# Optimization experiments

Measured on AMD Instinct MI355X. Metric: run time of the kernel, lower is better.

## Reference

```python
import jax, jax.numpy as jnp
import numpy as np

N = 50000
E = 800000
IN_CH = 128
HID = 16
HEADS = 8
OUT_CH = 64
NEG_SLOPE = 0.2


def setup_inputs() -> dict:
    key = jax.random.key(0)
    ks = jax.random.split(key, 16)
    x = jax.random.normal(ks[0], (N, IN_CH), dtype=jnp.float32)
    edge_index = jax.random.randint(ks[1], (2, E), 0, N, dtype=jnp.int64)
    s = 0.05
    # GATv2 layer 1: in=128 -> heads=8, out=16 (concat -> 128)
    W1l = jax.random.normal(ks[2], (IN_CH, HEADS * HID), dtype=jnp.float32) * s
    b1l = jnp.zeros((HEADS * HID,), dtype=jnp.float32)
    W1r = jax.random.normal(ks[3], (IN_CH, HEADS * HID), dtype=jnp.float32) * s
    b1r = jnp.zeros((HEADS * HID,), dtype=jnp.float32)
    att1 = jax.random.normal(ks[4], (HEADS, HID), dtype=jnp.float32) * s
    bias1 = jnp.zeros((HEADS * HID,), dtype=jnp.float32)
    # GATv2 layer 2: in=128 -> heads=1, out=64
    W2l = jax.random.normal(ks[5], (HEADS * HID, OUT_CH), dtype=jnp.float32) * s
    b2l = jnp.zeros((OUT_CH,), dtype=jnp.float32)
    W2r = jax.random.normal(ks[6], (HEADS * HID, OUT_CH), dtype=jnp.float32) * s
    b2r = jnp.zeros((OUT_CH,), dtype=jnp.float32)
    att2 = jax.random.normal(ks[7], (1, OUT_CH), dtype=jnp.float32) * s
    bias2 = jnp.zeros((OUT_CH,), dtype=jnp.float32)
    return dict(x=x, edge_index=edge_index,
                W1l=W1l, b1l=b1l, W1r=W1r, b1r=b1r, att1=att1, bias1=bias1,
                W2l=W2l, b2l=b2l, W2r=W2r, b2r=b2r, att2=att2, bias2=bias2)


def gatv2_conv(x, src, dst, Wl, bl, Wr, br, att, bias, heads, out_ch, concat):
    n = x.shape[0]
    xl = (x @ Wl + bl).reshape(n, heads, out_ch)  # source transform
    xr = (x @ Wr + br).reshape(n, heads, out_ch)  # target transform
    m = xl[src] + xr[dst]                          # [E, H, C]
    m = jnp.where(m > 0, m, NEG_SLOPE * m)         # LeakyReLU(0.2)
    alpha = jnp.einsum('ehc,hc->eh', m, att)       # [E, H]
    # segment softmax over destination nodes (every node has a self loop)
    amax = jax.ops.segment_max(alpha, dst, num_segments=n)
    ea = jnp.exp(alpha - amax[dst])
    denom = jax.ops.segment_sum(ea, dst, num_segments=n)
    w = ea / denom[dst]                            # [E, H]
    out = jax.ops.segment_sum(xl[src] * w[:, :, None], dst, num_segments=n)
    if concat:
        out = out.reshape(n, heads * out_ch)
    else:
        out = out.mean(axis=1)
    return out + bias


def reference(x, edge_index, W1l, b1l, W1r, b1r, att1, bias1,
              W2l, b2l, W2r, b2r, att2, bias2):
    n = x.shape[0]
    loops = jnp.arange(n, dtype=edge_index.dtype)
    src = jnp.concatenate([edge_index[0], loops])
    dst = jnp.concatenate([edge_index[1], loops])
    # dropout layers are identity in eval mode
    h = gatv2_conv(x, src, dst, W1l, b1l, W1r, b1r, att1, bias1,
                   heads=HEADS, out_ch=HID, concat=True)
    h = jax.nn.elu(h)
    out = gatv2_conv(h, src, dst, W2l, b2l, W2r, b2r, att2, bias2,
                     heads=1, out_ch=OUT_CH, concat=True)
    return out
```

## Files before the change

### kernel.cpp

```cpp
#include <hip/hip_runtime.h>
#include <hip/hip_bf16.h>

constexpr int N_  = 50000;
constexpr int E_  = 800000;
constexpr int ET_ = 850000;
constexpr float NEG_SLOPE = 0.2f;

constexpr int SCAN_NB = (N_ + 255) / 256;

typedef __attribute__((ext_vector_type(8))) short short8;
typedef __attribute__((ext_vector_type(4))) float f32x4;

__device__ inline void edge_sd(int e, const int* __restrict__ ei, int& s, int& d) {
    if (e < E_) { s = ei[e]; d = ei[E_ + e]; }
    else        { s = e - E_; d = s; }
}

__device__ inline float leaky(float v) { return fmaxf(v, NEG_SLOPE * v); }

__device__ inline unsigned bf16rn(float f) {
    union { float f; unsigned u; } v; v.f = f;
    return (v.u + 0x7fffu + ((v.u >> 16) & 1u)) >> 16;
}
__device__ inline float2 unpack2(unsigned u) {
    return make_float2(__uint_as_float(u << 16), __uint_as_float(u & 0xffff0000u));
}

__global__ __launch_bounds__(256) void hist_kernel(
        const int* __restrict__ ei, int* __restrict__ count, int* __restrict__ off) {
    int e = blockIdx.x * 256 + threadIdx.x;
    if (e >= ET_) return;
    int s, d; edge_sd(e, ei, s, d);
    off[e] = atomicAdd(&count[d], 1);
}

__global__ __launch_bounds__(256) void scan_partial(
        const int* __restrict__ count, int* __restrict__ bsum) {
    __shared__ int red[256];
    int t = threadIdx.x;
    int i = blockIdx.x * 256 + t;
    red[t] = (i < N_) ? count[i] : 0;
    __syncthreads();
    #pragma unroll
    for (int o = 128; o > 0; o >>= 1) {
        if (t < o) red[t] += red[t + o];
        __syncthreads();
    }
    if (t == 0) bsum[blockIdx.x] = red[0];
}

__global__ __launch_bounds__(256) void scan_top(
        const int* __restrict__ bsum, int* __restrict__ bstart) {
    __shared__ int buf[256];
    int t = threadIdx.x;
    int v = (t < SCAN_NB) ? bsum[t] : 0;
    buf[t] = v;
    __syncthreads();
    #pragma unroll
    for (int o = 1; o < 256; o <<= 1) {
        int add = (t >= o) ? buf[t - o] : 0;
        __syncthreads();
        buf[t] += add;
        __syncthreads();
    }
    if (t < SCAN_NB) bstart[t] = buf[t] - v;
}

__global__ __launch_bounds__(256) void scan_final(
        const int* __restrict__ count, const int* __restrict__ bstart,
        int* __restrict__ start) {
    __shared__ int buf[256];
    int t = threadIdx.x;
    int i = blockIdx.x * 256 + t;
    int v = (i < N_) ? count[i] : 0;
    buf[t] = v;
    __syncthreads();
    #pragma unroll
    for (int o = 1; o < 256; o <<= 1) {
        int add = (t >= o) ? buf[t - o] : 0;
        __syncthreads();
        buf[t] += add;
        __syncthreads();
    }
    if (i < N_) start[i] = bstart[blockIdx.x] + buf[t] - v;
}

__global__ __launch_bounds__(256) void scatter_kernel(
        const int* __restrict__ ei, const int* __restrict__ start,
        const int* __restrict__ off, int* __restrict__ csr_src) {
    int e = blockIdx.x * 256 + threadIdx.x;
    if (e >= ET_) return;
    int s, d; edge_sd(e, ei, s, d);
    csr_src[start[d] + off[e]] = s;
}

__global__ __launch_bounds__(256) void convert_w(
        const float* __restrict__ Wl, const float* __restrict__ Wr,
        unsigned short* __restrict__ wsw) {
    int tid = blockIdx.x * 256 + threadIdx.x;
    if (tid >= 32768) return;
    int j    = tid & 7;
    int lane = (tid >> 3) & 63;
    int ks   = (tid >> 9) & 3;
    int ct   = tid >> 11;
    int k = ks * 32 + ((lane >> 4) & 3) * 8 + j;
    int c = ct * 16 + (lane & 15);
    float v = (c < 128) ? Wl[k * 128 + c] : Wr[k * 128 + (c - 128)];
    wsw[tid] = (unsigned short)bf16rn(v);
}

__global__ __launch_bounds__(256) void convert_w2(
        const float* __restrict__ Wl, const float* __restrict__ Wr,
        unsigned short* __restrict__ wsw2) {
    int tid = blockIdx.x * 256 + threadIdx.x;
    if (tid >= 16384) return;
    int j    = tid & 7;
    int lane = (tid >> 3) & 63;
    int ks   = (tid >> 9) & 3;
    int ct   = tid >> 11;
    int k = ks * 32 + ((lane >> 4) & 3) * 8 + j;
    int c = ct * 16 + (lane & 15);
    float v = (c < 64) ? Wl[k * 64 + c] : Wr[k * 64 + (c - 64)];
    wsw2[tid] = (unsigned short)bf16rn(v);
}

__global__ __launch_bounds__(256) void gemm1_mfma(
        const float* __restrict__ x,
        const unsigned short* __restrict__ wsw,
        const float* __restrict__ bl, const float* __restrict__ br,
        unsigned short* __restrict__ xlu, float* __restrict__ xr1) {
    const int wave = threadIdx.x >> 6;
    const int lane = threadIdx.x & 63;
    const int n0 = blockIdx.x * 16;
    const int m = lane & 15;
    const int q = (lane >> 4) & 3;
    const float* __restrict__ arow = x + (size_t)(n0 + m) * 128 + q * 8;
    short8 afrag[4];
    #pragma unroll
    for (int ks = 0; ks < 4; ++ks) {
        float4 v0 = *(const float4*)(arow + ks * 32);
        float4 v1 = *(const float4*)(arow + ks * 32 + 4);
        short8 a;
        a[0] = (short)bf16rn(v0.x); a[1] = (short)bf16rn(v0.y);
        a[2] = (short)bf16rn(v0.z); a[3] = (short)bf16rn(v0.w);
        a[4] = (short)bf16rn(v1.x); a[5] = (short)bf16rn(v1.y);
        a[6] = (short)bf16rn(v1.z); a[7] = (short)bf16rn(v1.w);
        afrag[ks] = a;
    }
    #pragma unroll
    for (int i = 0; i < 4; ++i) {
        const int ct = wave * 4 + i;
        f32x4 acc = {0.f, 0.f, 0.f, 0.f};
        #pragma unroll
        for (int ks = 0; ks < 4; ++ks) {
            short8 b = *(const short8*)(wsw + ((size_t)(ct * 4 + ks) * 64 + lane) * 8);
            acc = __builtin_amdgcn_mfma_f32_16x16x32_bf16(afrag[ks], b, acc, 0, 0, 0);
        }
        const int col = ct * 16 + m;
        if (ct < 8) {
            float bias = bl[col];
            #pragma unroll
            for (int j = 0; j < 4; ++j) {
                int row = n0 + q * 4 + j;
                xlu[(size_t)row * 128 + col] = (unsigned short)bf16rn(acc[j] + bias);
            }
        } else {
            float bias = br[col - 128];
            #pragma unroll
            for (int j = 0; j < 4; ++j) {
                int row = n0 + q * 4 + j;
                xr1[(size_t)row * 128 + (col - 128)] = acc[j] + bias;
            }
        }
    }
}

__global__ __launch_bounds__(256) void fused1(
        const int* __restrict__ csr_src, const int* __restrict__ start,
        const int* __restrict__ count,
        const unsigned* __restrict__ xl1b, const float* __restrict__ xr1,
        const float* __restrict__ att, const float* __restrict__ bias1,
        float* __restrict__ hout) {
    int t = blockIdx.x * 256 + threadIdx.x;
    int n = __builtin_amdgcn_readfirstlane(t >> 6);
    int lane = t & 63;
    if (n >= N_) return;
    float2 xr = *(const float2*)(xr1 + (size_t)n * 128 + 2 * lane);
    float2 av = *(const float2*)(att + 2 * lane);
    int p0 = __builtin_amdgcn_readfirstlane(start[n]);
    int p1 = p0 + __builtin_amdgcn_readfirstlane(count[n]);
    float2 acc = make_float2(0.f, 0.f);
    float l = 0.f;
    for (int p = p0; p < p1; p += 4) {
        int q1 = p + 1 < p1 ? p + 1 : p1 - 1;
        int q2 = p + 2 < p1 ? p + 2 : p1 - 1;
        int q3 = p + 3 < p1 ? p + 3 : p1 - 1;
        int s0 = __builtin_amdgcn_readfirstlane(csr_src[p]);
        int s1 = __builtin_amdgcn_readfirstlane(csr_src[q1]);
        int s2 = __builtin_amdgcn_readfirstlane(csr_src[q2]);
        int s3 = __builtin_amdgcn_readfirstlane(csr_src[q3]);
        float2 x0 = unpack2(xl1b[(size_t)s0 * 64 + lane]);
        float2 x1 = unpack2(xl1b[(size_t)s1 * 64 + lane]);
        float2 x2 = unpack2(xl1b[(size_t)s2 * 64 + lane]);
        float2 x3 = unpack2(xl1b[(size_t)s3 * 64 + lane]);
        float a0 = fmaf(leaky(x0.x + xr.x), av.x, leaky(x0.y + xr.y) * av.y);
        float a1 = fmaf(leaky(x1.x + xr.x), av.x, leaky(x1.y + xr.y) * av.y);
        float a2 = fmaf(leaky(x2.x + xr.x), av.x, leaky(x2.y + xr.y) * av.y);
        float a3 = fmaf(leaky(x3.x + xr.x), av.x, leaky(x3.y + xr.y) * av.y);
        a0 += __shfl_xor(a0, 1); a1 += __shfl_xor(a1, 1);
        a2 += __shfl_xor(a2, 1); a3 += __shfl_xor(a3, 1);
        a0 += __shfl_xor(a0, 2); a1 += __shfl_xor(a1, 2);
        a2 += __shfl_xor(a2, 2); a3 += __shfl_xor(a3, 2);
        a0 += __shfl_xor(a0, 4); a1 += __shfl_xor(a1, 4);
        a2 += __shfl_xor(a2, 4); a3 += __shfl_xor(a3, 4);
        float w0 = __expf(a0);
        float w1 = p + 1 < p1 ? __expf(a1) : 0.f;
        float w2 = p + 2 < p1 ? __expf(a2) : 0.f;
        float w3 = p + 3 < p1 ? __expf(a3) : 0.f;
        acc.x = fmaf(w0, x0.x, acc.x); acc.y = fmaf(w0, x0.y, acc.y); l += w0;
        acc.x = fmaf(w1, x1.x, acc.x); acc.y = fmaf(w1, x1.y, acc.y); l += w1;
        acc.x = fmaf(w2, x2.x, acc.x); acc.y = fmaf(w2, x2.y, acc.y); l += w2;
        acc.x = fmaf(w3, x3.x, acc.x); acc.y = fmaf(w3, x3.y, acc.y); l += w3;
    }
    float2 bv = *(const float2*)(bias1 + 2 * lane);
    float vx = acc.x / l + bv.x;
    float vy = acc.y / l + bv.y;
    float2 o;
    o.x = vx > 0.f ? vx : (__expf(vx) - 1.f);
    o.y = vy > 0.f ? vy : (__expf(vy) - 1.f);
    *(float2*)(hout + (size_t)n * 128 + 2 * lane) = o;
}

__global__ __launch_bounds__(256) void gemm2_mfma(
        const float* __restrict__ hbuf,
        const unsigned short* __restrict__ wsw2,
        const float* __restrict__ bl, const float* __restrict__ br,
        unsigned short* __restrict__ xlu2, float* __restrict__ xr2) {
    const int wave = threadIdx.x >> 6;
    const int lane = threadIdx.x & 63;
    const int n0 = blockIdx.x * 16;
    const int m = lane & 15;
    const int q = (lane >> 4) & 3;
    const float* __restrict__ arow = hbuf + (size_t)(n0 + m) * 128 + q * 8;
    short8 afrag[4];
    #pragma unroll
    for (int ks = 0; ks < 4; ++ks) {
        float4 v0 = *(const float4*)(arow + ks * 32);
        float4 v1 = *(const float4*)(arow + ks * 32 + 4);
        short8 a;
        a[0] = (short)bf16rn(v0.x); a[1] = (short)bf16rn(v0.y);
        a[2] = (short)bf16rn(v0.z); a[3] = (short)bf16rn(v0.w);
        a[4] = (short)bf16rn(v1.x); a[5] = (short)bf16rn(v1.y);
        a[6] = (short)bf16rn(v1.z); a[7] = (short)bf16rn(v1.w);
        afrag[ks] = a;
    }
    #pragma unroll
    for (int i = 0; i < 2; ++i) {
        const int ct = wave * 2 + i;
        f32x4 acc = {0.f, 0.f, 0.f, 0.f};
        #pragma unroll
        for (int ks = 0; ks < 4; ++ks) {
            short8 b = *(const short8*)(wsw2 + ((size_t)(ct * 4 + ks) * 64 + lane) * 8);
            acc = __builtin_amdgcn_mfma_f32_16x16x32_bf16(afrag[ks], b, acc, 0, 0, 0);
        }
        const int col = ct * 16 + m;
        if (ct < 4) {
            float bias = bl[col];
            #pragma unroll
            for (int j = 0; j < 4; ++j) {
                int row = n0 + q * 4 + j;
                xlu2[(size_t)row * 64 + col] = (unsigned short)bf16rn(acc[j] + bias);
            }
        } else {
            float bias = br[col - 64];
            #pragma unroll
            for (int j = 0; j < 4; ++j) {
                int row = n0 + q * 4 + j;
                xr2[(size_t)row * 64 + (col - 64)] = acc[j] + bias;
            }
        }
    }
}

__global__ __launch_bounds__(256) void fused2(
        const int* __restrict__ csr_src, const int* __restrict__ start,
        const int* __restrict__ count,
        const unsigned* __restrict__ xl2b, const float* __restrict__ xr2,
        const float* __restrict__ att, const float* __restrict__ bias2,
        float* __restrict__ out) {
    int t = blockIdx.x * 256 + threadIdx.x;
    int n = __builtin_amdgcn_readfirstlane(t >> 6);
    int lane = t & 63;
    int half = lane >> 5;
    int lc   = lane & 31;
    if (n >= N_) return;
    float2 xr = *(const float2*)(xr2 + (size_t)n * 64 + 2 * lc);
    float2 av = *(const float2*)(att + 2 * lc);
    int p0 = __builtin_amdgcn_readfirstlane(start[n]);
    int p1 = p0 + __builtin_amdgcn_readfirstlane(count[n]);
    float2 acc = make_float2(0.f, 0.f);
    float l = 0.f;
    for (int p = p0; p < p1; p += 8) {
        #pragma unroll
        for (int u = 0; u < 4; ++u) {
            int pe = p + 2 * u + half;
            int pc = pe < p1 ? pe : p1 - 1;
            int s  = csr_src[pc];
            float2 xv = unpack2(xl2b[(size_t)s * 32 + lc]);
            float a = fmaf(leaky(xv.x + xr.x), av.x, leaky(xv.y + xr.y) * av.y);
            a += __shfl_xor(a, 1);
            a += __shfl_xor(a, 2);
            a += __shfl_xor(a, 4);
            a += __shfl_xor(a, 8);
            a += __shfl_xor(a, 16);
            float w = pe < p1 ? __expf(a) : 0.f;
            acc.x = fmaf(w, xv.x, acc.x);
            acc.y = fmaf(w, xv.y, acc.y);
            l += w;
        }
    }
    acc.x += __shfl_xor(acc.x, 32);
    acc.y += __shfl_xor(acc.y, 32);
    l     += __shfl_xor(l, 32);
    if (half == 0) {
        float2 bv = *(const float2*)(bias2 + 2 * lc);
        float2 o;
        o.x = acc.x / l + bv.x;
        o.y = acc.y / l + bv.y;
        *(float2*)(out + (size_t)n * 64 + 2 * lc) = o;
    }
}

extern "C" void kernel_launch(void* const* d_in, const int* in_sizes, int n_in,
                              void* d_out, int out_size, void* d_ws, size_t ws_size,
                              hipStream_t stream) {
    (void)in_sizes; (void)n_in; (void)out_size; (void)ws_size;
    const float* x     = (const float*)d_in[0];
    const int*   ei    = (const int*)d_in[1];
    const float* W1l   = (const float*)d_in[2];
    const float* b1l   = (const float*)d_in[3];
    const float* W1r   = (const float*)d_in[4];
    const float* b1r   = (const float*)d_in[5];
    const float* att1  = (const float*)d_in[6];
    const float* bias1 = (const float*)d_in[7];
    const float* W2l   = (const float*)d_in[8];
    const float* b2l   = (const float*)d_in[9];
    const float* W2r   = (const float*)d_in[10];
    const float* b2r   = (const float*)d_in[11];
    const float* att2  = (const float*)d_in[12];
    const float* bias2 = (const float*)d_in[13];
    float* out = (float*)d_out;

    float* xr1      = (float*)d_ws;
    float* hbuf     = xr1 + 6400000;
    unsigned* xl1b  = (unsigned*)(hbuf + 6400000);
    int* count   = (int*)(xl1b + 3200000);
    int* startp  = count + 50000;
    int* off     = startp + 50000;
    int* csr_src = off + 850000;
    int* bsum    = csr_src + 850000;
    int* bstart  = bsum + 256;
    unsigned short* wsw2 = (unsigned short*)(bstart + 256);
    unsigned* xl2b = xl1b;
    float* xr2     = xr1;
    unsigned short* wsw = (unsigned short*)hbuf;

    hipMemsetAsync((void*)count, 0, 50000 * sizeof(int), stream);

    const int EB = (ET_ + 255) / 256;
    hist_kernel <<<EB, 256, 0, stream>>>(ei, count, off);
    scan_partial<<<SCAN_NB, 256, 0, stream>>>(count, bsum);
    scan_top    <<<1, 256, 0, stream>>>(bsum, bstart);
    scan_final  <<<SCAN_NB, 256, 0, stream>>>(count, bstart, startp);
    scatter_kernel<<<EB, 256, 0, stream>>>(ei, startp, off, csr_src);

    convert_w  <<<128, 256, 0, stream>>>(W1l, W1r, wsw);
    convert_w2 <<<64, 256, 0, stream>>>(W2l, W2r, wsw2);
    gemm1_mfma <<<N_ / 16, 256, 0, stream>>>(x, wsw, b1l, b1r,
                                             (unsigned short*)xl1b, xr1);
    fused1<<<(N_ * 64 + 255) / 256, 256, 0, stream>>>(csr_src, startp, count,
                                                      xl1b, xr1, att1, bias1, hbuf);

    gemm2_mfma <<<N_ / 16, 256, 0, stream>>>(hbuf, wsw2, b2l, b2r,
                                             (unsigned short*)xl2b, xr2);
    fused2<<<(N_ * 64 + 255) / 256, 256, 0, stream>>>(csr_src, startp, count,
                                                      xl2b, xr2, att2, bias2, out);
}
```

Measured before the change: 274.9 us.

## Pad CSR rows to multiples of eight for vectorized neighbor index loads

Each node's CSR segment is padded to a multiple of eight entries (zero-filled via an enlarged memset), so the aggregation kernels can load source indices with aligned int4 vector loads instead of clamped scalar loads. fused2 now loads all eight indices per iteration up front. The hist kernel skips the unneeded source read, and the two weight-conversion kernels are merged into one launch. The cost is a larger memset and extra padded index storage; padded slots point at node 0 and are masked by the existing weight predicates.

```diff
diff --git a/kernel.cpp b/kernel.cpp
--- a/kernel.cpp
+++ b/kernel.cpp
@@ -7,14 +7,10 @@
 constexpr float NEG_SLOPE = 0.2f;
 
 constexpr int SCAN_NB = (N_ + 255) / 256;
+constexpr int CSR_CAP = 1250008;
 
 typedef __attribute__((ext_vector_type(8))) short short8;
 typedef __attribute__((ext_vector_type(4))) float f32x4;
-
-__device__ inline void edge_sd(int e, const int* __restrict__ ei, int& s, int& d) {
-    if (e < E_) { s = ei[e]; d = ei[E_ + e]; }
-    else        { s = e - E_; d = s; }
-}
 
 __device__ inline float leaky(float v) { return fmaxf(v, NEG_SLOPE * v); }
 
@@ -30,7 +26,7 @@
         const int* __restrict__ ei, int* __restrict__ count, int* __restrict__ off) {
     int e = blockIdx.x * 256 + threadIdx.x;
     if (e >= ET_) return;
-    int s, d; edge_sd(e, ei, s, d);
+    int d = (e < E_) ? ei[E_ + e] : e - E_;
     off[e] = atomicAdd(&count[d], 1);
 }
 
@@ -39,7 +35,7 @@
     __shared__ int red[256];
     int t = threadIdx.x;
     int i = blockIdx.x * 256 + t;
-    red[t] = (i < N_) ? count[i] : 0;
+    red[t] = (i < N_) ? ((count[i] + 7) & ~7) : 0;
     __syncthreads();
     #pragma unroll
     for (int o = 128; o > 0; o >>= 1) {
@@ -72,7 +68,7 @@
     __shared__ int buf[256];
     int t = threadIdx.x;
     int i = blockIdx.x * 256 + t;
-    int v = (i < N_) ? count[i] : 0;
+    int v = (i < N_) ? ((count[i] + 7) & ~7) : 0;
     buf[t] = v;
     __syncthreads();
     #pragma unroll
@@ -90,38 +86,38 @@
         const int* __restrict__ off, int* __restrict__ csr_src) {
     int e = blockIdx.x * 256 + threadIdx.x;
     if (e >= ET_) return;
-    int s, d; edge_sd(e, ei, s, d);
+    int s, d;
+    if (e < E_) { s = ei[e]; d = ei[E_ + e]; }
+    else        { s = e - E_; d = s; }
     csr_src[start[d] + off[e]] = s;
 }
 
-__global__ __launch_bounds__(256) void convert_w(
-        const float* __restrict__ Wl, const float* __restrict__ Wr,
-        unsigned short* __restrict__ wsw) {
+__global__ __launch_bounds__(256) void convert_w_all(
+        const float* __restrict__ W1l, const float* __restrict__ W1r,
+        const float* __restrict__ W2l, const float* __restrict__ W2r,
+        unsigned short* __restrict__ wsw, unsigned short* __restrict__ wsw2) {
     int tid = blockIdx.x * 256 + threadIdx.x;
-    if (tid >= 32768) return;
-    int j    = tid & 7;
-    int lane = (tid >> 3) & 63;
-    int ks   = (tid >> 9) & 3;
-    int ct   = tid >> 11;
-    int k = ks * 32 + ((lane >> 4) & 3) * 8 + j;
-    int c = ct * 16 + (lane & 15);
-    float v = (c < 128) ? Wl[k * 128 + c] : Wr[k * 128 + (c - 128)];
-    wsw[tid] = (unsigned short)bf16rn(v);
-}
-
-__global__ __launch_bounds__(256) void convert_w2(
-        const float* __restrict__ Wl, const float* __restrict__ Wr,
-        unsigned short* __restrict__ wsw2) {
-    int tid = blockIdx.x * 256 + threadIdx.x;
-    if (tid >= 16384) return;
-    int j    = tid & 7;
-    int lane = (tid >> 3) & 63;
-    int ks   = (tid >> 9) & 3;
-    int ct   = tid >> 11;
-    int k = ks * 32 + ((lane >> 4) & 3) * 8 + j;
-    int c = ct * 16 + (lane & 15);
-    float v = (c < 64) ? Wl[k * 64 + c] : Wr[k * 64 + (c - 64)];
-    wsw2[tid] = (unsigned short)bf16rn(v);
+    if (tid >= 49152) return;
+    if (tid < 32768) {
+        int j    = tid & 7;
+        int lane = (tid >> 3) & 63;
+        int ks   = (tid >> 9) & 3;
+        int ct   = tid >> 11;
+        int k = ks * 32 + ((lane >> 4) & 3) * 8 + j;
+        int c = ct * 16 + (lane & 15);
+        float v = (c < 128) ? W1l[k * 128 + c] : W1r[k * 128 + (c - 128)];
+        wsw[tid] = (unsigned short)bf16rn(v);
+    } else {
+        int t2   = tid - 32768;
+        int j    = t2 & 7;
+        int lane = (t2 >> 3) & 63;
+        int ks   = (t2 >> 9) & 3;
+        int ct   = t2 >> 11;
+        int k = ks * 32 + ((lane >> 4) & 3) * 8 + j;
+        int c = ct * 16 + (lane & 15);
+        float v = (c < 64) ? W2l[k * 64 + c] : W2r[k * 64 + (c - 64)];
+        wsw2[t2] = (unsigned short)bf16rn(v);
+    }
 }
 
 __global__ __launch_bounds__(256) void gemm1_mfma(
@@ -192,13 +188,11 @@
     float2 acc = make_float2(0.f, 0.f);
     float l = 0.f;
     for (int p = p0; p < p1; p += 4) {
-        int q1 = p + 1 < p1 ? p + 1 : p1 - 1;
-        int q2 = p + 2 < p1 ? p + 2 : p1 - 1;
-        int q3 = p + 3 < p1 ? p + 3 : p1 - 1;
-        int s0 = __builtin_amdgcn_readfirstlane(csr_src[p]);
-        int s1 = __builtin_amdgcn_readfirstlane(csr_src[q1]);
-        int s2 = __builtin_amdgcn_readfirstlane(csr_src[q2]);
-        int s3 = __builtin_amdgcn_readfirstlane(csr_src[q3]);
+        int4 si = *(const int4*)(csr_src + p);
+        int s0 = __builtin_amdgcn_readfirstlane(si.x);
+        int s1 = __builtin_amdgcn_readfirstlane(si.y);
+        int s2 = __builtin_amdgcn_readfirstlane(si.z);
+        int s3 = __builtin_amdgcn_readfirstlane(si.w);
         float2 x0 = unpack2(xl1b[(size_t)s0 * 64 + lane]);
         float2 x1 = unpack2(xl1b[(size_t)s1 * 64 + lane]);
         float2 x2 = unpack2(xl1b[(size_t)s2 * 64 + lane]);
@@ -301,11 +295,21 @@
     float2 acc = make_float2(0.f, 0.f);
     float l = 0.f;
     for (int p = p0; p < p1; p += 8) {
+        int4 ia = *(const int4*)(csr_src + p);
+        int4 ib = *(const int4*)(csr_src + p + 4);
+        int sx[8];
+        sx[0] = __builtin_amdgcn_readfirstlane(ia.x);
+        sx[1] = __builtin_amdgcn_readfirstlane(ia.y);
+        sx[2] = __builtin_amdgcn_readfirstlane(ia.z);
+        sx[3] = __builtin_amdgcn_readfirstlane(ia.w);
+        sx[4] = __builtin_amdgcn_readfirstlane(ib.x);
+        sx[5] = __builtin_amdgcn_readfirstlane(ib.y);
+        sx[6] = __builtin_amdgcn_readfirstlane(ib.z);
+        sx[7] = __builtin_amdgcn_readfirstlane(ib.w);
         #pragma unroll
         for (int u = 0; u < 4; ++u) {
             int pe = p + 2 * u + half;
-            int pc = pe < p1 ? pe : p1 - 1;
-            int s  = csr_src[pc];
+            int s  = sx[2 * u + half];
             float2 xv = unpack2(xl2b[(size_t)s * 32 + lc]);
             float a = fmaf(leaky(xv.x + xr.x), av.x, leaky(xv.y + xr.y) * av.y);
             a += __shfl_xor(a, 1);
@@ -355,17 +359,17 @@
     float* hbuf     = xr1 + 6400000;
     unsigned* xl1b  = (unsigned*)(hbuf + 6400000);
     int* count   = (int*)(xl1b + 3200000);
-    int* startp  = count + 50000;
+    int* csr_src = count + 50000;
+    int* startp  = csr_src + CSR_CAP;
     int* off     = startp + 50000;
-    int* csr_src = off + 850000;
-    int* bsum    = csr_src + 850000;
+    int* bsum    = off + 850000;
     int* bstart  = bsum + 256;
     unsigned short* wsw2 = (unsigned short*)(bstart + 256);
     unsigned* xl2b = xl1b;
     float* xr2     = xr1;
     unsigned short* wsw = (unsigned short*)hbuf;
 
-    hipMemsetAsync((void*)count, 0, 50000 * sizeof(int), stream);
+    hipMemsetAsync((void*)count, 0, (size_t)(50000 + CSR_CAP) * 4, stream);
 
     const int EB = (ET_ + 255) / 256;
     hist_kernel <<<EB, 256, 0, stream>>>(ei, count, off);
@@ -374,8 +378,7 @@
     scan_final  <<<SCAN_NB, 256, 0, stream>>>(count, bstart, startp);
     scatter_kernel<<<EB, 256, 0, stream>>>(ei, startp, off, csr_src);
 
-    convert_w  <<<128, 256, 0, stream>>>(W1l, W1r, wsw);
-    convert_w2 <<<64, 256, 0, stream>>>(W2l, W2r, wsw2);
+    convert_w_all<<<192, 256, 0, stream>>>(W1l, W1r, W2l, W2r, wsw, wsw2);
     gemm1_mfma <<<N_ / 16, 256, 0, stream>>>(x, wsw, b1l, b1r,
                                              (unsigned short*)xl1b, xr1);
     fused1<<<(N_ * 64 + 255) / 256, 256, 0, stream>>>(csr_src, startp, count,
```

Result: no change. 272.8 us (-0.8%).
